# Optimization experiments

Hardware: AMD Instinct MI355X
Metric: run time of the kernel (lower is better)

## Reference

```python
import jax, jax.numpy as jnp
import numpy as np

B, N, K = 4, 8192, 16
FEAT = 512
GRID = 45
M = GRID * GRID


def _p(key, shape, scale=0.05):
    return jax.random.normal(key, shape, dtype=jnp.float32) * scale


def setup_inputs() -> dict:
    key = jax.random.key(0)
    ks = jax.random.split(key, 40)
    inp = {"pts": jax.random.normal(ks[0], (B, N, 3), dtype=jnp.float32)}
    specs = {
        "w1": (64, 12), "b1": (64,), "w2": (64, 64), "b2": (64,), "w3": (64, 64), "b3": (64,),
        "g1a": (64, 64), "g1ab": (64,), "g1b": (128, 64), "g1bb": (128,),
        "g2a": (128, 128), "g2ab": (128,), "g2b": (1024, 128), "g2bb": (1024,),
        "m1": (FEAT, 1024), "m1b": (FEAT,), "m2": (FEAT, FEAT), "m2b": (FEAT,),
        "f1a": (FEAT, FEAT + 2), "f1ab": (FEAT,), "f1b": (FEAT, FEAT), "f1bb": (FEAT,), "f1c": (3, FEAT), "f1cb": (3,),
        "f2a": (FEAT, FEAT + 3), "f2ab": (FEAT,), "f2b": (FEAT, FEAT), "f2bb": (FEAT,), "f2c": (3, FEAT), "f2cb": (3,),
    }
    for i, (name, shp) in enumerate(specs.items()):
        inp[name] = _p(ks[i + 1], shp)
    return inp


def conv1x1(x, w, b):
    # x: (B,C,N), w: (Cout,Cin), b: (Cout,)
    return jnp.einsum('bcn,oc->bon', x, w) + b[None, :, None]


def knn_idx(x, k):
    # x: (B,C,N) -> neighbor indices (B,N,k) by smallest squared distance (self included)
    xt = jnp.swapaxes(x, 1, 2)                      # (B,N,C)
    sq = jnp.sum(xt * xt, axis=-1)                  # (B,N)
    inner = jnp.einsum('bnc,bmc->bnm', xt, xt)      # (B,N,N)
    neg_d2 = 2.0 * inner - sq[:, :, None] - sq[:, None, :]
    return jax.lax.top_k(neg_d2, k)[1]


def gather_nbrs(feats_t, idx):
    # feats_t: (B,N,C), idx: (B,N,k) -> (B,N,k,C)
    return jax.vmap(lambda f, i: f[i])(feats_t, idx)


def local_maxpool(x, idx):
    # x: (B,C,N) -> (B,C,N) max over k neighbors
    nb = gather_nbrs(jnp.swapaxes(x, 1, 2), idx)    # (B,N,k,C)
    return jnp.swapaxes(jnp.max(nb, axis=2), 1, 2)


def local_cov(pts_t, idx):
    # pts_t: (B,3,N) -> (B,12,N): coords + outer product of first two neighbors
    p = jnp.swapaxes(pts_t, 1, 2)                   # (B,N,3)
    nb = gather_nbrs(p, idx)                        # (B,N,k,3)
    outer = nb[:, :, 0, :, None] * nb[:, :, 1, None, :]   # (B,N,3,3)
    feat = jnp.concatenate([p, outer.reshape(p.shape[0], p.shape[1], 9)], axis=-1)
    return jnp.swapaxes(feat, 1, 2)


def _forward(pts, w1, b1, w2, b2, w3, b3, g1a, g1ab, g1b, g1bb, g2a, g2ab, g2b, g2bb,
             m1, m1b, m2, m2b, f1a, f1ab, f1b, f1bb, f1c, f1cb, f2a, f2ab, f2b, f2bb, f2c, f2cb):
    relu = jax.nn.relu
    pts_t = jnp.swapaxes(pts, 1, 2)                 # (B,3,N)
    # ---- encoder ----
    idx = knn_idx(pts_t, K)
    x = local_cov(pts_t, idx)                       # (B,12,N)
    x = relu(conv1x1(x, w1, b1))
    x = relu(conv1x1(x, w2, b2))
    x = relu(conv1x1(x, w3, b3))                    # (B,64,N)
    idx = knn_idx(x, K)
    g = local_maxpool(x, idx)
    g = conv1x1(relu(conv1x1(g, g1a, g1ab)), g1b, g1bb)   # (B,128,N)
    idx = knn_idx(g, K)
    h = local_maxpool(g, idx)
    h = conv1x1(relu(conv1x1(h, g2a, g2ab)), g2b, g2bb)   # (B,1024,N)
    glob = jnp.max(h, axis=2, keepdims=True)        # (B,1024,1)
    code = conv1x1(relu(conv1x1(glob, m1, m1b)), m2, m2b)  # (B,FEAT,1)
    # ---- decoder ----
    Bs = code.shape[0]
    cw = jnp.broadcast_to(code, (Bs, FEAT, M))
    lin = jnp.linspace(-0.3, 0.3, GRID, dtype=jnp.float32)
    gx, gy = jnp.meshgrid(lin, lin, indexing='ij')
    grid = jnp.stack([gx.ravel(), gy.ravel()], axis=0)     # (2,M)
    grid = jnp.broadcast_to(grid[None], (Bs, 2, M))

    def fold(points, wa, ba, wb, bb, wc, bc):
        y = jnp.concatenate([cw, points], axis=1)
        y = relu(conv1x1(y, wa, ba))
        y = relu(conv1x1(y, wb, bb))
        return conv1x1(y, wc, bc)                    # (B,3,M)

    mid = fold(grid, f1a, f1ab, f1b, f1bb, f1c, f1cb)
    rec = fold(mid, f2a, f2ab, f2b, f2bb, f2c, f2cb)
    return jnp.swapaxes(rec, 1, 2)                   # (B,M,3)


def reference(pts, w1, b1, w2, b2, w3, b3, g1a, g1ab, g1b, g1bb, g2a, g2ab, g2b, g2bb,
              m1, m1b, m2, m2b, f1a, f1ab, f1b, f1bb, f1c, f1cb, f2a, f2ab, f2b, f2bb, f2c, f2cb):
    return _forward(pts, w1, b1, w2, b2, w3, b3, g1a, g1ab, g1b, g1bb, g2a, g2ab, g2b, g2bb,
                    m1, m1b, m2, m2b, f1a, f1ab, f1b, f1bb, f1c, f1cb, f2a, f2ab, f2b, f2bb, f2c, f2cb)
```

## Files before the change

kernel.cpp:

```cpp
#include <hip/hip_runtime.h>
#include <stdint.h>

#define B_ 4
#define N_ 8192
#define K_ 16
#define FEAT_ 512
#define GRID_ 45
#define M_ (GRID_*GRID_)

typedef unsigned long long ull;
typedef __bf16 bf16x8 __attribute__((ext_vector_type(8)));
typedef float f32x16 __attribute__((ext_vector_type(16)));


__device__ __forceinline__ unsigned int fmap(float f){
  unsigned int u = __float_as_uint(f);
  return (u & 0x80000000u) ? ~u : (u | 0x80000000u);
}
__device__ __forceinline__ float funmap(unsigned int u){
  return (u & 0x80000000u) ? __uint_as_float(u ^ 0x80000000u) : __uint_as_float(~u);
}

__device__ __forceinline__ void ins16(ull (&d)[16], ull k){
  if (k < d[15]){
    bool c[16];
#pragma unroll
    for (int s = 0; s < 16; ++s) c[s] = k < d[s];
#pragma unroll
    for (int s = 15; s >= 1; --s) d[s] = c[s-1] ? d[s-1] : (c[s] ? k : d[s]);
    if (c[0]) d[0] = k;
  }
}

#define GLDS16(l, g) __builtin_amdgcn_global_load_lds((const __attribute__((address_space(1))) void*)(g), (__attribute__((address_space(3))) void*)(l), 16, 0, 0)
#define GLDS4(l, g)  __builtin_amdgcn_global_load_lds((const __attribute__((address_space(1))) void*)(g), (__attribute__((address_space(3))) void*)(l), 4, 0, 0)

#define KEY_INF 0xFF800000FFFFFFFFull

__global__ void k_init(unsigned int* glob){
  int i = blockIdx.x*256 + threadIdx.x;
  if (i < B_*1024) glob[i] = 0x007FFFFFu;
}

__global__ __launch_bounds__(256) void k_nn1(const float* __restrict__ pts,
                                             unsigned long long* __restrict__ nn64){
  __shared__ float sp[2048*3];
  int b = blockIdx.z, s = blockIdx.y;
  int c0 = s*2048;
  const float* P = pts + (size_t)b*N_*3;
  for (int i = threadIdx.x; i < 2048*3; i += 256) sp[i] = P[c0*3 + i];
  __syncthreads();
  int n = blockIdx.x*256 + threadIdx.x;
  float qx = P[n*3], qy = P[n*3+1], qz = P[n*3+2];
  float best = 1e30f; int bi = 0;
  for (int j = 0; j < 2048; ++j){
    float dx = qx - sp[j*3], dy = qy - sp[j*3+1], dz = qz - sp[j*3+2];
    float d2 = fmaf(dx,dx, fmaf(dy,dy, dz*dz));
    int cj = c0 + j;
    if (d2 < best && cj != n){ best = d2; bi = cj; }
  }
  unsigned long long key = ((unsigned long long)__float_as_uint(best) << 32) | (unsigned int)bi;
  atomicMin(&nn64[(size_t)b*N_ + n], key);
}

__global__ __launch_bounds__(256) void k_cov_mlp(const float* __restrict__ pts,
    const unsigned long long* __restrict__ nn64,
    const float* __restrict__ w1, const float* __restrict__ b1,
    const float* __restrict__ w2, const float* __restrict__ b2,
    const float* __restrict__ w3, const float* __restrict__ b3,
    float* __restrict__ xout){
  __shared__ __align__(16) float W1t[12*64];
  __shared__ __align__(16) float W2t[64*64];
  __shared__ __align__(16) float W3t[64*64];
  __shared__ float B1[64], B2[64], B3[64];
  __shared__ __align__(16) float x0[64][12];
  __shared__ __align__(16) float h1[64][64];
  __shared__ __align__(16) float h2[64][64];
  int b = blockIdx.y; int n0 = blockIdx.x*64; int tid = threadIdx.x;
  for (int i = tid; i < 12*64; i += 256){ int o = i % 64, ci = i / 64; W1t[i] = w1[o*12 + ci]; }
  for (int i = tid; i < 64*64; i += 256){ int o = i % 64, ci = i / 64; W2t[i] = w2[o*64 + ci]; W3t[i] = w3[o*64 + ci]; }
  if (tid < 64){ B1[tid]=b1[tid]; B2[tid]=b2[tid]; B3[tid]=b3[tid]; }
  {
    int p = tid % 64, cg = tid / 64;
    int n = n0 + p;
    const float* P = pts + ((size_t)b*N_ + n)*3;
    int nb = (int)(nn64[(size_t)b*N_ + n] & 0xFFFFFFFFull);
    const float* Q = pts + ((size_t)b*N_ + nb)*3;
    if (cg == 0){ x0[p][0]=P[0]; x0[p][1]=P[1]; x0[p][2]=P[2]; }
    else { int i = cg-1; float pi = P[i];
      x0[p][3+i*3+0]=pi*Q[0]; x0[p][3+i*3+1]=pi*Q[1]; x0[p][3+i*3+2]=pi*Q[2]; }
  }
  __syncthreads();
  { int o = tid % 64, pg = tid / 64;
    for (int p = pg; p < 64; p += 4){
      float acc = B1[o];
#pragma unroll
      for (int ci = 0; ci < 12; ++ci) acc = fmaf(W1t[ci*64+o], x0[p][ci], acc);
      h1[p][o] = fmaxf(acc, 0.f);
    } }
  __syncthreads();
  { int o = tid % 64, pg = tid / 64;
    for (int p = pg; p < 64; p += 4){
      float acc = B2[o];
#pragma unroll
      for (int ci = 0; ci < 64; ++ci) acc = fmaf(W2t[ci*64+o], h1[p][ci], acc);
      h2[p][o] = fmaxf(acc, 0.f);
    } }
  __syncthreads();
  { int o = tid % 64, pg = tid / 64;
    for (int p = pg; p < 64; p += 4){
      float acc = B3[o];
#pragma unroll
      for (int ci = 0; ci < 64; ++ci) acc = fmaf(W3t[ci*64+o], h2[p][ci], acc);
      xout[((size_t)b*N_ + n0 + p)*64 + o] = fmaxf(acc, 0.f);
    } }
}

template<int KF>
__global__ __launch_bounds__(256) void k_prep4(const float* __restrict__ f,
    unsigned short* __restrict__ T, float* __restrict__ cc){
  int b = blockIdx.y; int n = blockIdx.x*256 + threadIdx.x;
  const float* src = f + ((size_t)b*N_ + n)*(KF*16);
  char* Tb = (char*)T;
  float ss = 0.f;
#pragma unroll
  for (int kf = 0; kf < KF; ++kf){
    float v[16];
#pragma unroll
    for (int c4 = 0; c4 < 4; ++c4){
      float4 t4 = *(const float4*)&src[kf*16 + c4*4];
      v[c4*4]=t4.x; v[c4*4+1]=t4.y; v[c4*4+2]=t4.z; v[c4*4+3]=t4.w;
    }
    unsigned short hs[16], ls[16];
#pragma unroll
    for (int c = 0; c < 16; ++c){
      float x = v[c];
      ss = fmaf(x, x, ss);
      __bf16 h = (__bf16)x;
      __bf16 l = (__bf16)(x - (float)h);
      hs[c] = __builtin_bit_cast(unsigned short, h);
      ls[c] = __builtin_bit_cast(unsigned short, l);
    }
    size_t base = ((((size_t)b*KF + kf)*2)*2)*(size_t)(N_*16) + (size_t)n*16;
    const size_t HS = (size_t)N_*16;
    const size_t PS = 2*HS;
    *(uint4*)(Tb + base)            = *(uint4*)&hs[0];
    *(uint4*)(Tb + base + HS)       = *(uint4*)&hs[8];
    *(uint4*)(Tb + base + PS)       = *(uint4*)&ls[0];
    *(uint4*)(Tb + base + PS + HS)  = *(uint4*)&ls[8];
  }
  cc[(size_t)b*N_ + n] = ss;
}

template<int KF, int MW, int S>
__global__ __launch_bounds__(256, MW) void k_knnF(const unsigned short* __restrict__ T,
    const float* __restrict__ ccg, ull* __restrict__ qkeys){
  extern __shared__ char smem[];
  constexpr int NT = (N_/S)/64;
  char* As = smem;
  char* Cs = smem + KF*4096;

  const int tid = threadIdx.x, lane = tid & 63, wid = tid >> 6;
  const int hi = lane >> 5, l31 = lane & 31;
  const int b = blockIdx.z, sp = blockIdx.y, q0 = blockIdx.x*128;
  const int c0 = sp*(N_/S);
  const char* Tb = (const char*)T;
  const size_t HS = (size_t)N_*16, PS = 2*HS, KS = 4*HS;
  const size_t Bb = (size_t)b*KF*KS;
  const float* ccb = ccg + (size_t)b*N_;

  const int q = q0 + wid*32 + l31;
  bf16x8 qh[KF], ql[KF];
#pragma unroll
  for (int kf = 0; kf < KF; ++kf){
    size_t o = Bb + kf*KS + hi*HS + (size_t)q*16;
    qh[kf] = *(const bf16x8*)(Tb + o);
    ql[kf] = *(const bf16x8*)(Tb + o + PS);
  }

  ull keys[16];
#pragma unroll
  for (int t = 0; t < 16; ++t) keys[t] = KEY_INF;
  float kapf = __builtin_inff();

  auto stage = [&](int t0){
#pragma unroll
    for (int si = 0; si < KF; ++si){
      int s = wid + 4*si;
      int kf = s >> 2, pl = (s >> 1) & 1, h = s & 1;
      GLDS16(As + s*1024,
             Tb + Bb + kf*KS + pl*PS + h*HS + (size_t)(c0 + t0)*16);
    }
    if (wid == 0) GLDS4(Cs, (const char*)(ccb + c0 + t0));
  };

  for (int t = 0; t < NT; ++t){
    const int t0 = t*64;
    __syncthreads();
    stage(t0);
    asm volatile("s_waitcnt vmcnt(0)" ::: "memory");
    __syncthreads();

    const char* Ab = As + hi*1024 + l31*16;
    const float* cct = (const float*)Cs;
#pragma unroll
    for (int i = 0; i < 2; ++i){
      f32x16 acc = (f32x16)(0.f);
#pragma unroll
      for (int kf = 0; kf < KF; ++kf){
        bf16x8 ah = *(const bf16x8*)(Ab + kf*4096 + i*512);
        bf16x8 al = *(const bf16x8*)(Ab + kf*4096 + 2048 + i*512);
        acc = __builtin_amdgcn_mfma_f32_32x32x16_bf16(ah, qh[kf], acc, 0, 0, 0);
        acc = __builtin_amdgcn_mfma_f32_32x32x16_bf16(ah, ql[kf], acc, 0, 0, 0);
        acc = __builtin_amdgcn_mfma_f32_32x32x16_bf16(al, qh[kf], acc, 0, 0, 0);
      }
#pragma unroll
      for (int rq = 0; rq < 4; ++rq){
        float4 c4 = *(const float4*)(cct + i*32 + 4*hi + 8*rq);
        int rowb = c0 + t0 + i*32 + 4*hi + 8*rq;
        float v0 = fmaf(-2.f, acc[rq*4+0], c4.x);
        float v1 = fmaf(-2.f, acc[rq*4+1], c4.y);
        float v2 = fmaf(-2.f, acc[rq*4+2], c4.z);
        float v3 = fmaf(-2.f, acc[rq*4+3], c4.w);
        if (fminf(fminf(v0, v1), fminf(v2, v3)) <= kapf){
          if (v0 <= kapf) ins16(keys, ((ull)fmap(v0) << 32) | (unsigned)(rowb+0));
          if (v1 <= kapf) ins16(keys, ((ull)fmap(v1) << 32) | (unsigned)(rowb+1));
          if (v2 <= kapf) ins16(keys, ((ull)fmap(v2) << 32) | (unsigned)(rowb+2));
          if (v3 <= kapf) ins16(keys, ((ull)fmap(v3) << 32) | (unsigned)(rowb+3));
          kapf = funmap((unsigned)(keys[15] >> 32));
        }
      }
    }
  }
  ull* op = qkeys + (((size_t)((size_t)b*N_ + q)*S + sp)*2 + hi)*16;
#pragma unroll
  for (int t = 0; t < 16; ++t) op[t] = keys[t];
}

template<int S>
__global__ void k_sel(const ull* __restrict__ qkeys, int* __restrict__ idxout){
  int i = blockIdx.x*256 + threadIdx.x;
  if (i >= B_*N_) return;
  ull best[16];
#pragma unroll
  for (int t = 0; t < 16; ++t) best[t] = KEY_INF;
  const ull* kp = qkeys + (size_t)i*(S*32);
  for (int t = 0; t < S*32; ++t) ins16(best, kp[t]);
  int* op = idxout + (size_t)i*16;
#pragma unroll
  for (int t = 0; t < 16; ++t) op[t] = (int)(best[t] & 0xffffffffu);
}

__global__ __launch_bounds__(256) void k_gpool_mlp(const float* __restrict__ x,
    const int* __restrict__ idx,
    const float* __restrict__ g1a, const float* __restrict__ g1ab,
    const float* __restrict__ g1b, const float* __restrict__ g1bb,
    float* __restrict__ gout){
  __shared__ __align__(16) float Wt1[64*64];
  __shared__ __align__(16) float Wt2[64*128];
  __shared__ float Ba[64], Bb[128];
  __shared__ __align__(16) float m[64][64];
  __shared__ __align__(16) float r[64][64];
  int b = blockIdx.y; int n0 = blockIdx.x*64; int tid = threadIdx.x;
  for (int i = tid; i < 64*64; i += 256){ int o = i%64, ci = i/64; Wt1[i] = g1a[o*64+ci]; }
  for (int i = tid; i < 64*128; i += 256){ int o = i%128, ci = i/128; Wt2[i] = g1b[o*64+ci]; }
  if (tid < 64) Ba[tid] = g1ab[tid];
  if (tid < 128) Bb[tid] = g1bb[tid];
  { int p = tid/4, cg = tid%4; int n = n0 + p;
    const int* ip = idx + ((size_t)b*N_ + n)*16;
    float mm[16];
#pragma unroll
    for (int u = 0; u < 16; ++u) mm[u] = -1e30f;
    for (int k = 0; k < 16; ++k){
      int nb = ip[k];
      const float4* src = (const float4*)(x + ((size_t)b*N_ + nb)*64 + cg*16);
#pragma unroll
      for (int u = 0; u < 4; ++u){
        float4 v = src[u];
        mm[4*u  ] = fmaxf(mm[4*u  ], v.x); mm[4*u+1] = fmaxf(mm[4*u+1], v.y);
        mm[4*u+2] = fmaxf(mm[4*u+2], v.z); mm[4*u+3] = fmaxf(mm[4*u+3], v.w);
      }
    }
#pragma unroll
    for (int u = 0; u < 16; ++u) m[p][cg*16+u] = mm[u];
  }
  __syncthreads();
  { int o = tid%64, pg = tid/64;
    float acc[16];
#pragma unroll
    for (int u = 0; u < 16; ++u) acc[u] = Ba[o];
    for (int ci = 0; ci < 64; ci += 4){
      float w0 = Wt1[ci*64+o], w1_ = Wt1[(ci+1)*64+o], w2_ = Wt1[(ci+2)*64+o], w3_ = Wt1[(ci+3)*64+o];
#pragma unroll
      for (int u = 0; u < 16; ++u){
        float4 mv = *(const float4*)&m[pg*16+u][ci];
        acc[u] = fmaf(w0, mv.x, acc[u]); acc[u] = fmaf(w1_, mv.y, acc[u]);
        acc[u] = fmaf(w2_, mv.z, acc[u]); acc[u] = fmaf(w3_, mv.w, acc[u]);
      }
    }
#pragma unroll
    for (int u = 0; u < 16; ++u) r[pg*16+u][o] = fmaxf(acc[u], 0.f);
  }
  __syncthreads();
  { int o = tid%128, pg = tid/128;
    float acc[32];
#pragma unroll
    for (int u = 0; u < 32; ++u) acc[u] = Bb[o];
    for (int ci = 0; ci < 64; ci += 4){
      float w0 = Wt2[ci*128+o], w1_ = Wt2[(ci+1)*128+o], w2_ = Wt2[(ci+2)*128+o], w3_ = Wt2[(ci+3)*128+o];
#pragma unroll
      for (int u = 0; u < 32; ++u){
        float4 rv = *(const float4*)&r[pg*32+u][ci];
        acc[u] = fmaf(w0, rv.x, acc[u]); acc[u] = fmaf(w1_, rv.y, acc[u]);
        acc[u] = fmaf(w2_, rv.z, acc[u]); acc[u] = fmaf(w3_, rv.w, acc[u]);
      }
    }
#pragma unroll
    for (int u = 0; u < 32; ++u)
      gout[((size_t)b*N_ + n0 + pg*32 + u)*128 + o] = acc[u];
  }
}

__global__ __launch_bounds__(256) void k_hpool_max(const float* __restrict__ g,
    const int* __restrict__ idx,
    const float* __restrict__ g2a, const float* __restrict__ g2ab,
    const float* __restrict__ g2b, const float* __restrict__ g2bb,
    unsigned int* __restrict__ glob){
  __shared__ __align__(16) float m[32][128];
  __shared__ __align__(16) float t[32][128];
  int b = blockIdx.y; int n0 = blockIdx.x*32; int tid = threadIdx.x;
  { int p = tid/8, cg = tid%8; int n = n0+p;
    const int* ip = idx + ((size_t)b*N_+n)*16;
    float mm[16];
#pragma unroll
    for (int u = 0; u < 16; ++u) mm[u] = -1e30f;
    for (int k = 0; k < 16; ++k){
      int nb = ip[k];
      const float4* src = (const float4*)(g + ((size_t)b*N_+nb)*128 + cg*16);
#pragma unroll
      for (int u = 0; u < 4; ++u){
        float4 v = src[u];
        mm[4*u  ] = fmaxf(mm[4*u  ], v.x); mm[4*u+1] = fmaxf(mm[4*u+1], v.y);
        mm[4*u+2] = fmaxf(mm[4*u+2], v.z); mm[4*u+3] = fmaxf(mm[4*u+3], v.w);
      }
    }
#pragma unroll
    for (int u = 0; u < 16; ++u) m[p][cg*16+u] = mm[u];
  }
  __syncthreads();
  { int o = tid%128, pg = tid/128;
    float acc[16];
#pragma unroll
    for (int u = 0; u < 16; ++u) acc[u] = g2ab[o];
    const float4* wrow = (const float4*)(g2a + (size_t)o*128);
    for (int c4 = 0; c4 < 32; ++c4){
      float4 wv = wrow[c4];
#pragma unroll
      for (int u = 0; u < 16; ++u){
        float4 mv = *(const float4*)&m[pg*16+u][c4*4];
        acc[u] = fmaf(wv.x,mv.x,acc[u]); acc[u] = fmaf(wv.y,mv.y,acc[u]);
        acc[u] = fmaf(wv.z,mv.z,acc[u]); acc[u] = fmaf(wv.w,mv.w,acc[u]);
      }
    }
#pragma unroll
    for (int u = 0; u < 16; ++u) t[pg*16+u][o] = fmaxf(acc[u], 0.f);
  }
  __syncthreads();
  for (int oc = 0; oc < 4; ++oc){
    int o = oc*256 + tid;
    const float4* wrow = (const float4*)(g2b + (size_t)o*128);
    float acc[32];
#pragma unroll
    for (int u = 0; u < 32; ++u) acc[u] = 0.f;
    for (int c4 = 0; c4 < 32; ++c4){
      float4 wv = wrow[c4];
#pragma unroll
      for (int u = 0; u < 32; ++u){
        float4 tv = *(const float4*)&t[u][c4*4];
        acc[u] = fmaf(wv.x,tv.x,acc[u]); acc[u] = fmaf(wv.y,tv.y,acc[u]);
        acc[u] = fmaf(wv.z,tv.z,acc[u]); acc[u] = fmaf(wv.w,tv.w,acc[u]);
      }
    }
    float bias = g2bb[o];
    float mx = -1e30f;
#pragma unroll
    for (int u = 0; u < 32; ++u) mx = fmaxf(mx, acc[u] + bias);
    atomicMax(&glob[b*1024 + o], fmap(mx));
  }
}

__global__ __launch_bounds__(512) void k_code(const unsigned int* __restrict__ glob,
    const float* __restrict__ m1, const float* __restrict__ m1b,
    const float* __restrict__ m2, const float* __restrict__ m2b,
    const float* __restrict__ f1a, const float* __restrict__ f1ab,
    const float* __restrict__ f2a, const float* __restrict__ f2ab,
    float* __restrict__ base1, float* __restrict__ base2){
  __shared__ __align__(16) float gl_s[1024];
  __shared__ __align__(16) float hid_s[512];
  __shared__ __align__(16) float code_s[512];
  int b = blockIdx.x; int tid = threadIdx.x;
  for (int i = tid; i < 1024; i += 512) gl_s[i] = funmap(glob[b*1024+i]);
  __syncthreads();
  { float acc = m1b[tid];
    const float4* wr = (const float4*)(m1 + (size_t)tid*1024);
    for (int c4 = 0; c4 < 256; ++c4){ float4 wv = wr[c4]; float4 gv = *(const float4*)&gl_s[c4*4];
      acc = fmaf(wv.x,gv.x,acc); acc = fmaf(wv.y,gv.y,acc);
      acc = fmaf(wv.z,gv.z,acc); acc = fmaf(wv.w,gv.w,acc); }
    hid_s[tid] = fmaxf(acc, 0.f);
  }
  __syncthreads();
  { float acc = m2b[tid];
    const float4* wr = (const float4*)(m2 + (size_t)tid*512);
    for (int c4 = 0; c4 < 128; ++c4){ float4 wv = wr[c4]; float4 hv = *(const float4*)&hid_s[c4*4];
      acc = fmaf(wv.x,hv.x,acc); acc = fmaf(wv.y,hv.y,acc);
      acc = fmaf(wv.z,hv.z,acc); acc = fmaf(wv.w,hv.w,acc); }
    code_s[tid] = acc;
  }
  __syncthreads();
  { float acc = f1ab[tid];
    const float* wr = f1a + (size_t)tid*514;
    for (int c = 0; c < 512; ++c) acc = fmaf(wr[c], code_s[c], acc);
    base1[b*512 + tid] = acc;
  }
  { float acc = f2ab[tid];
    const float* wr = f2a + (size_t)tid*515;
    for (int c = 0; c < 512; ++c) acc = fmaf(wr[c], code_s[c], acc);
    base2[b*512 + tid] = acc;
  }
}

template<int NIN>
__global__ __launch_bounds__(256) void k_fold(const float* __restrict__ base,
    const float* __restrict__ fa,
    const float* __restrict__ fb, const float* __restrict__ fbb,
    const float* __restrict__ fc, const float* __restrict__ fcb,
    const float* __restrict__ pin, float* __restrict__ pout){
  __shared__ __align__(16) float y1[32][512];
  __shared__ __align__(16) float y2[32][516];
  __shared__ float pcoord[32][NIN];
  int b = blockIdx.y; int m0 = blockIdx.x*32; int tid = threadIdx.x;
  if (tid < 32*NIN){
    int p = tid / NIN, c = tid % NIN;
    int mm = min(m0 + p, M_-1);
    float v;
    if (NIN == 2){
      const float step = 0.6f/44.f;
      int ii = (c == 0) ? (mm/GRID_) : (mm%GRID_);
      v = -0.3f + step*ii;
    } else {
      v = pin[((size_t)b*M_ + mm)*3 + c];
    }
    pcoord[p][c] = v;
  }
  __syncthreads();
  const int stride_a = 512 + NIN;
  for (int rep = 0; rep < 2; ++rep){
    int o = rep*256 + tid;
    float av[NIN];
#pragma unroll
    for (int c = 0; c < NIN; ++c) av[c] = fa[(size_t)o*stride_a + 512 + c];
    float bv = base[b*512 + o];
    for (int p = 0; p < 32; ++p){
      float acc = bv;
#pragma unroll
      for (int c = 0; c < NIN; ++c) acc = fmaf(av[c], pcoord[p][c], acc);
      y1[p][o] = fmaxf(acc, 0.f);
    }
  }
  __syncthreads();
  for (int rep = 0; rep < 2; ++rep){
    int o2 = rep*256 + tid;
    const float* wr = fb + (size_t)o2*512;
    float acc[32];
#pragma unroll
    for (int u = 0; u < 32; ++u) acc[u] = 0.f;
    for (int c4 = 0; c4 < 128; ++c4){
      float4 wv = *(const float4*)&wr[c4*4];
#pragma unroll
      for (int u = 0; u < 32; ++u){
        float4 yv = *(const float4*)&y1[u][c4*4];
        acc[u] = fmaf(wv.x,yv.x,acc[u]); acc[u] = fmaf(wv.y,yv.y,acc[u]);
        acc[u] = fmaf(wv.z,yv.z,acc[u]); acc[u] = fmaf(wv.w,yv.w,acc[u]);
      }
    }
    float bias = fbb[o2];
#pragma unroll
    for (int u = 0; u < 32; ++u) y2[u][o2] = fmaxf(acc[u] + bias, 0.f);
  }
  __syncthreads();
  if (tid < 96){
    int p = tid / 3, c = tid % 3;
    const float* wr = fc + (size_t)c*512;
    float acc = fcb[c];
    for (int o4 = 0; o4 < 128; ++o4){
      float4 wv = *(const float4*)&wr[o4*4];
      float4 yv = *(const float4*)&y2[p][o4*4];
      acc = fmaf(wv.x,yv.x,acc); acc = fmaf(wv.y,yv.y,acc);
      acc = fmaf(wv.z,yv.z,acc); acc = fmaf(wv.w,yv.w,acc);
    }
    int mm = m0 + p;
    if (mm < M_) pout[((size_t)b*M_ + mm)*3 + c] = acc;
  }
}

extern "C" void kernel_launch(void* const* d_in, const int* in_sizes, int n_in,
                              void* d_out, int out_size, void* d_ws, size_t ws_size,
                              hipStream_t stream){
  const float* pts  = (const float*)d_in[0];
  const float* w1   = (const float*)d_in[1];  const float* b1   = (const float*)d_in[2];
  const float* w2   = (const float*)d_in[3];  const float* b2   = (const float*)d_in[4];
  const float* w3   = (const float*)d_in[5];  const float* b3   = (const float*)d_in[6];
  const float* g1a  = (const float*)d_in[7];  const float* g1ab = (const float*)d_in[8];
  const float* g1b  = (const float*)d_in[9];  const float* g1bb = (const float*)d_in[10];
  const float* g2a  = (const float*)d_in[11]; const float* g2ab = (const float*)d_in[12];
  const float* g2b  = (const float*)d_in[13]; const float* g2bb = (const float*)d_in[14];
  const float* m1   = (const float*)d_in[15]; const float* m1b  = (const float*)d_in[16];
  const float* m2   = (const float*)d_in[17]; const float* m2b  = (const float*)d_in[18];
  const float* f1a  = (const float*)d_in[19]; const float* f1ab = (const float*)d_in[20];
  const float* f1b  = (const float*)d_in[21]; const float* f1bb = (const float*)d_in[22];
  const float* f1c  = (const float*)d_in[23]; const float* f1cb = (const float*)d_in[24];
  const float* f2a  = (const float*)d_in[25]; const float* f2ab = (const float*)d_in[26];
  const float* f2b  = (const float*)d_in[27]; const float* f2bb = (const float*)d_in[28];
  const float* f2c  = (const float*)d_in[29]; const float* f2cb = (const float*)d_in[30];
  float* out = (float*)d_out;

  char* w = (char*)d_ws;
  auto alloc = [&](size_t bytes){ char* p = w; w += (bytes + 255) & ~(size_t)255; return p; };
  unsigned long long* nn64 = (unsigned long long*)alloc((size_t)B_*N_*8);
  float* x    = (float*)alloc((size_t)B_*N_*64*4);
  float* g    = (float*)alloc((size_t)B_*N_*128*4);
  unsigned short* T64  = (unsigned short*)alloc((size_t)B_*4*4*N_*16);
  unsigned short* T128 = (unsigned short*)alloc((size_t)B_*8*4*N_*16);
  float* ccf  = (float*)alloc((size_t)B_*N_*4);
  int*   idx  = (int*)alloc((size_t)B_*N_*16*4);
  ull*   qkeys = (ull*)alloc((size_t)B_*N_*4*2*16*8);
  unsigned int* glob = (unsigned int*)alloc((size_t)B_*1024*4);
  float* base1 = (float*)alloc((size_t)B_*512*4);
  float* base2 = (float*)alloc((size_t)B_*512*4);
  float* mid   = (float*)alloc((size_t)B_*M_*3*4);
  (void)ws_size; (void)in_sizes; (void)n_in; (void)out_size;

  const int SMEM4 = 4*4096 + 256;
  const int SMEM8 = 8*4096 + 256;
  hipFuncSetAttribute((const void*)k_knnF<4,4,4>, hipFuncAttributeMaxDynamicSharedMemorySize, SMEM4);
  hipFuncSetAttribute((const void*)k_knnF<8,3,4>, hipFuncAttributeMaxDynamicSharedMemorySize, SMEM8);

  hipMemsetAsync(nn64, 0xFF, (size_t)B_*N_*8, stream);
  k_init<<<dim3((B_*1024+255)/256), 256, 0, stream>>>(glob);
  k_nn1<<<dim3(N_/256, 4, B_), 256, 0, stream>>>(pts, nn64);
  k_cov_mlp<<<dim3(N_/64, B_), 256, 0, stream>>>(pts, nn64, w1,b1,w2,b2,w3,b3, x);

  k_prep4<4><<<dim3(N_/256, B_), 256, 0, stream>>>(x, T64, ccf);
  k_knnF<4,4,4><<<dim3(N_/128, 4, B_), 256, SMEM4, stream>>>(T64, ccf, qkeys);
  k_sel<4><<<dim3(B_*N_/256), 256, 0, stream>>>(qkeys, idx);

  k_gpool_mlp<<<dim3(N_/64, B_), 256, 0, stream>>>(x, idx, g1a,g1ab,g1b,g1bb, g);

  k_prep4<8><<<dim3(N_/256, B_), 256, 0, stream>>>(g, T128, ccf);
  k_knnF<8,3,4><<<dim3(N_/128, 4, B_), 256, SMEM8, stream>>>(T128, ccf, qkeys);
  k_sel<4><<<dim3(B_*N_/256), 256, 0, stream>>>(qkeys, idx);

  k_hpool_max<<<dim3(N_/32, B_), 256, 0, stream>>>(g, idx, g2a,g2ab,g2b,g2bb, glob);
  k_code<<<dim3(B_), 512, 0, stream>>>(glob, m1,m1b,m2,m2b, f1a,f1ab, f2a,f2ab, base1, base2);
  k_fold<2><<<dim3((M_+31)/32, B_), 256, 0, stream>>>(base1, f1a, f1b, f1bb, f1c, f1cb, nullptr, mid);
  k_fold<3><<<dim3((M_+31)/32, B_), 256, 0, stream>>>(base2, f2a, f2b, f2bb, f2c, f2cb, mid, out);
}
```

Baseline: 1.832 ms.

## Buffer KNN candidates in per-thread LDS queue and drain in wave-uniform batches

Inside the fused distance+top-k kernel, candidates that pass the threshold are now appended to a small per-thread LDS queue instead of being inserted into the sorted 16-entry register list right away. The queue is drained with batched insertions whenever any lane in the wave holds more than four entries, which cuts down on divergent per-element insertion branches. On the first tile the threshold is skipped and all values are inserted directly to seed the list. The cost is an extra 16KB of LDS per block, which may lower occupancy, plus a stale threshold between drains that lets more candidates through.

```diff
diff --git a/kernel.cpp b/kernel.cpp
--- a/kernel.cpp
+++ b/kernel.cpp
@@ -159,6 +159,7 @@
   constexpr int NT = (N_/S)/64;
   char* As = smem;
   char* Cs = smem + KF*4096;
+  ull*  Ps = (ull*)(smem + KF*4096 + 256);
 
   const int tid = threadIdx.x, lane = tid & 63, wid = tid >> 6;
   const int hi = lane >> 5, l31 = lane & 31;
@@ -182,6 +183,18 @@
 #pragma unroll
   for (int t = 0; t < 16; ++t) keys[t] = KEY_INF;
   float kapf = __builtin_inff();
+  ull* qls = Ps + tid*8;
+  int cnt = 0;
+
+  auto drain = [&](){
+    ull bq[8];
+#pragma unroll
+    for (int t = 0; t < 8; ++t) bq[t] = qls[t];
+#pragma unroll
+    for (int t = 0; t < 8; ++t) if (t < cnt) ins16(keys, bq[t]);
+    cnt = 0;
+    kapf = funmap((unsigned)(keys[15] >> 32));
+  };
 
   auto stage = [&](int t0){
 #pragma unroll
@@ -214,24 +227,36 @@
         acc = __builtin_amdgcn_mfma_f32_32x32x16_bf16(ah, ql[kf], acc, 0, 0, 0);
         acc = __builtin_amdgcn_mfma_f32_32x32x16_bf16(al, qh[kf], acc, 0, 0, 0);
       }
-#pragma unroll
-      for (int rq = 0; rq < 4; ++rq){
-        float4 c4 = *(const float4*)(cct + i*32 + 4*hi + 8*rq);
-        int rowb = c0 + t0 + i*32 + 4*hi + 8*rq;
-        float v0 = fmaf(-2.f, acc[rq*4+0], c4.x);
-        float v1 = fmaf(-2.f, acc[rq*4+1], c4.y);
-        float v2 = fmaf(-2.f, acc[rq*4+2], c4.z);
-        float v3 = fmaf(-2.f, acc[rq*4+3], c4.w);
-        if (fminf(fminf(v0, v1), fminf(v2, v3)) <= kapf){
-          if (v0 <= kapf) ins16(keys, ((ull)fmap(v0) << 32) | (unsigned)(rowb+0));
-          if (v1 <= kapf) ins16(keys, ((ull)fmap(v1) << 32) | (unsigned)(rowb+1));
-          if (v2 <= kapf) ins16(keys, ((ull)fmap(v2) << 32) | (unsigned)(rowb+2));
-          if (v3 <= kapf) ins16(keys, ((ull)fmap(v3) << 32) | (unsigned)(rowb+3));
-          kapf = funmap((unsigned)(keys[15] >> 32));
+      if (t == 0){
+#pragma unroll
+        for (int rq = 0; rq < 4; ++rq){
+          float4 c4 = *(const float4*)(cct + i*32 + 4*hi + 8*rq);
+          int rowb = c0 + i*32 + 4*hi + 8*rq;
+          ins16(keys, ((ull)fmap(fmaf(-2.f, acc[rq*4+0], c4.x)) << 32) | (unsigned)(rowb+0));
+          ins16(keys, ((ull)fmap(fmaf(-2.f, acc[rq*4+1], c4.y)) << 32) | (unsigned)(rowb+1));
+          ins16(keys, ((ull)fmap(fmaf(-2.f, acc[rq*4+2], c4.z)) << 32) | (unsigned)(rowb+2));
+          ins16(keys, ((ull)fmap(fmaf(-2.f, acc[rq*4+3], c4.w)) << 32) | (unsigned)(rowb+3));
         }
-      }
-    }
-  }
+        kapf = funmap((unsigned)(keys[15] >> 32));
+      } else {
+#pragma unroll
+        for (int rq = 0; rq < 4; ++rq){
+          float4 c4 = *(const float4*)(cct + i*32 + 4*hi + 8*rq);
+          int rowb = c0 + t0 + i*32 + 4*hi + 8*rq;
+          float v0 = fmaf(-2.f, acc[rq*4+0], c4.x);
+          float v1 = fmaf(-2.f, acc[rq*4+1], c4.y);
+          float v2 = fmaf(-2.f, acc[rq*4+2], c4.z);
+          float v3 = fmaf(-2.f, acc[rq*4+3], c4.w);
+          if (v0 <= kapf){ qls[cnt] = ((ull)fmap(v0) << 32) | (unsigned)(rowb+0); ++cnt; }
+          if (v1 <= kapf){ qls[cnt] = ((ull)fmap(v1) << 32) | (unsigned)(rowb+1); ++cnt; }
+          if (v2 <= kapf){ qls[cnt] = ((ull)fmap(v2) << 32) | (unsigned)(rowb+2); ++cnt; }
+          if (v3 <= kapf){ qls[cnt] = ((ull)fmap(v3) << 32) | (unsigned)(rowb+3); ++cnt; }
+          if (__any(cnt > 4)) drain();
+        }
+      }
+    }
+  }
+  drain();
   ull* op = qkeys + (((size_t)((size_t)b*N_ + q)*S + sp)*2 + hi)*16;
 #pragma unroll
   for (int t = 0; t < 16; ++t) op[t] = keys[t];
@@ -540,8 +565,8 @@
   float* mid   = (float*)alloc((size_t)B_*M_*3*4);
   (void)ws_size; (void)in_sizes; (void)n_in; (void)out_size;
 
-  const int SMEM4 = 4*4096 + 256;
-  const int SMEM8 = 8*4096 + 256;
+  const int SMEM4 = 4*4096 + 256 + 256*8*8;
+  const int SMEM8 = 8*4096 + 256 + 256*8*8;
   hipFuncSetAttribute((const void*)k_knnF<4,4,4>, hipFuncAttributeMaxDynamicSharedMemorySize, SMEM4);
   hipFuncSetAttribute((const void*)k_knnF<8,3,4>, hipFuncAttributeMaxDynamicSharedMemorySize, SMEM8);
 
```

New measurement: 2.713 ms. 48.1% more time.
